# Kernel optimization log

Measured on AMD Instinct MI355X. Metric: run time of the kernel, lower is better.

## Reference

```python
import jax, jax.numpy as jnp
import numpy as np

N = 10000; E = 320000; B = 262144
F_NODE = 64; F_EDGE = 8; H = 4; C = 32
EVO_IN = C * 4 * H + 1      # 513
EVO_HID = 256; EVO_DIM = 64
FLOW_IN = EVO_DIM + 5       # 69
FLOW_HID = 256
SLOPE = 0.01                # torch LeakyReLU default slope
GAT_SLOPE = 0.2             # GATv2 attention LeakyReLU slope
EPS = 1e-5                  # BatchNorm eps


def setup_inputs() -> dict:
    key = jax.random.key(0)
    ks = iter(jax.random.split(key, 64))
    def nrm(shape, scale=1.0):
        return jax.random.normal(next(ks), shape, jnp.float32) * scale
    inp = {}
    inp['x1'] = nrm((N, F_NODE))
    inp['edge_index1'] = jax.random.randint(next(ks), (2, E), 0, N)
    inp['edge_attr1'] = nrm((E, F_EDGE))
    inp['x2'] = nrm((N, F_NODE))
    inp['edge_index2'] = jax.random.randint(next(ks), (2, E), 0, N)
    inp['edge_attr2'] = nrm((E, F_EDGE))
    inp['dist_m'] = jax.random.uniform(next(ks), (N, N), jnp.float32)
    inp['node_visit'] = jax.random.uniform(next(ks), (N, 2), jnp.float32)
    inp['od_nodes'] = jax.random.randint(next(ks), (B, 2), 0, N)
    # GATv2Conv params per snapshot: lin_l, lin_r (bias=True), lin_edge (bias=False), att [H,C], out bias [H*C]
    for p in ('g1', 'g2'):
        s = 1.0 / np.sqrt(F_NODE)
        inp[p + '_Wl'] = nrm((H * C, F_NODE), s)
        inp[p + '_bl'] = jnp.zeros((H * C,), jnp.float32)
        inp[p + '_Wr'] = nrm((H * C, F_NODE), s)
        inp[p + '_br'] = jnp.zeros((H * C,), jnp.float32)
        inp[p + '_We'] = nrm((H * C, F_EDGE), 1.0 / np.sqrt(F_EDGE))
        inp[p + '_att'] = nrm((H, C), 1.0 / np.sqrt(C))
        inp[p + '_bias'] = jnp.zeros((H * C,), jnp.float32)
    # EvoEmbedding (all Linear bias=False)
    inp['e_W1'] = nrm((EVO_HID, EVO_IN), 1.0 / np.sqrt(EVO_IN))
    inp['e_W2'] = nrm((EVO_HID, EVO_HID), 1.0 / np.sqrt(EVO_HID))
    inp['e_W3'] = nrm((EVO_HID, EVO_HID), 1.0 / np.sqrt(EVO_HID))
    inp['e_W4'] = nrm((EVO_HID // 2, EVO_HID), 1.0 / np.sqrt(EVO_HID))
    inp['e_Wout'] = nrm((EVO_DIM, EVO_HID // 2), 1.0 / np.sqrt(EVO_HID // 2))
    # FlowGenerator (Linear bias=False) + BatchNorm affine params
    inp['f_W1'] = nrm((FLOW_HID, FLOW_IN), 1.0 / np.sqrt(FLOW_IN))
    inp['f_W2'] = nrm((FLOW_HID, FLOW_HID), 1.0 / np.sqrt(FLOW_HID))
    inp['f_W3'] = nrm((FLOW_HID, FLOW_HID), 1.0 / np.sqrt(FLOW_HID))
    inp['f_W4'] = nrm((FLOW_HID // 2, FLOW_HID), 1.0 / np.sqrt(FLOW_HID))
    inp['f_Wout'] = nrm((1, FLOW_HID // 2), 1.0 / np.sqrt(FLOW_HID // 2))
    inp['f_g1'] = jnp.ones((FLOW_HID,), jnp.float32);  inp['f_b1'] = jnp.zeros((FLOW_HID,), jnp.float32)
    inp['f_g2'] = jnp.ones((FLOW_HID,), jnp.float32);  inp['f_b2'] = jnp.zeros((FLOW_HID,), jnp.float32)
    inp['f_g3'] = jnp.ones((FLOW_HID,), jnp.float32);  inp['f_b3'] = jnp.zeros((FLOW_HID,), jnp.float32)
    inp['f_g4'] = jnp.ones((FLOW_HID // 2,), jnp.float32); inp['f_b4'] = jnp.zeros((FLOW_HID // 2,), jnp.float32)
    return inp


def _gatv2(x, ei, ea, Wl, bl, Wr, br, We, att, bias):
    src, dst = ei[0], ei[1]
    # self-loops with fill_value='mean': per-target mean of incoming edge_attr
    deg = jax.ops.segment_sum(jnp.ones_like(dst, jnp.float32), dst, N)
    mean_attr = jax.ops.segment_sum(ea, dst, N) / jnp.maximum(deg, 1.0)[:, None]
    loops = jnp.arange(N)
    s = jnp.concatenate([src, loops]); d = jnp.concatenate([dst, loops])
    eaf = jnp.concatenate([ea, mean_attr], axis=0)            # [E+N, F_EDGE]
    xl = (x @ Wl.T + bl).reshape(N, H, C)                     # source transform
    xr = (x @ Wr.T + br).reshape(N, H, C)                     # target transform
    em = (eaf @ We.T).reshape(-1, H, C)
    msg = jax.nn.leaky_relu(xl[s] + xr[d] + em, GAT_SLOPE)    # [E+N, H, C]
    scr = jnp.einsum('ehc,hc->eh', msg, att)                  # [E+N, H]
    mx = jax.ops.segment_max(scr, d, N)
    ex = jnp.exp(scr - mx[d])
    den = jax.ops.segment_sum(ex, d, N)
    alpha = ex / den[d]                                       # softmax over incoming edges
    out = jax.ops.segment_sum(alpha[:, :, None] * xl[s], d, N).reshape(N, H * C) + bias
    return jax.nn.relu(out), alpha


def _evo(v, W1, W2, W3, W4, Wout):
    h = jax.nn.leaky_relu(v @ W1.T, SLOPE)
    h = jax.nn.leaky_relu(h @ W2.T, SLOPE)
    h = jax.nn.leaky_relu(h @ W3.T, SLOPE)
    h = jax.nn.leaky_relu(h @ W4.T, SLOPE)
    return h @ Wout.T


def _bn(x, g, b):
    mu = x.mean(0)
    var = x.var(0)
    return (x - mu) * jax.lax.rsqrt(var + EPS) * g + b


def _flow(v, W1, W2, W3, W4, Wout, g1, b1, g2, b2, g3, b3, g4, b4):
    h = jax.nn.leaky_relu(_bn(v @ W1.T, g1, b1), SLOPE)
    h = jax.nn.leaky_relu(_bn(h @ W2.T, g2, b2), SLOPE)
    h = jax.nn.leaky_relu(_bn(h @ W3.T, g3, b3), SLOPE)
    h = jax.nn.leaky_relu(_bn(h @ W4.T, g4, b4), SLOPE)
    return (h @ Wout.T).squeeze(-1)


def reference(x1, edge_index1, edge_attr1, x2, edge_index2, edge_attr2, dist_m, node_visit, od_nodes,
              g1_Wl, g1_bl, g1_Wr, g1_br, g1_We, g1_att, g1_bias,
              g2_Wl, g2_bl, g2_Wr, g2_br, g2_We, g2_att, g2_bias,
              e_W1, e_W2, e_W3, e_W4, e_Wout,
              f_W1, f_W2, f_W3, f_W4, f_Wout,
              f_g1, f_b1, f_g2, f_b2, f_g3, f_b3, f_g4, f_b4):
    n1, a1 = _gatv2(x1, edge_index1, edge_attr1, g1_Wl, g1_bl, g1_Wr, g1_br, g1_We, g1_att, g1_bias)
    n2, a2 = _gatv2(x2, edge_index2, edge_attr2, g2_Wl, g2_bl, g2_Wr, g2_br, g2_We, g2_att, g2_bias)
    o = od_nodes[:, 0]; dn = od_nodes[:, 1]
    dist = dist_m[o, dn][:, None]                              # fused gather replacing python loop
    feat = jnp.concatenate([n1[o], n1[dn], n2[o], n2[dn], dist], axis=1)  # [B, 513]
    evo = _evo(feat, e_W1, e_W2, e_W3, e_W4, e_Wout)           # [B, EVO_DIM]
    # NOTE: original uses node_visit[:,0] for BOTH o_visit and d_visit (kept faithful)
    ov = node_visit[o, 0:1]; dv = node_visit[dn, 0:1]
    ovn = node_visit[o, 1:2]; dvn = node_visit[dn, 1:2]
    cat = jnp.concatenate([evo, ov, dv, ovn, dvn, dist], axis=1)  # [B, 69]
    inferred = _flow(cat, f_W1, f_W2, f_W3, f_W4, f_Wout, f_g1, f_b1, f_g2, f_b2, f_g3, f_b3, f_g4, f_b4)
    return (inferred, a1, a2, evo)
```

## Files before the change

### kernel.cpp

```cpp
#include <hip/hip_runtime.h>

typedef unsigned short u16;
typedef unsigned int u32;

#define NN 10000
#define NE 320000
#define ET 330000
#define NB 262144

typedef __attribute__((ext_vector_type(8))) short bf16x8;
typedef __attribute__((ext_vector_type(4))) float f32x4;

__device__ __forceinline__ u16 f2b(float f) {
  u32 u = __float_as_uint(f);
  u += 0x7fffu + ((u >> 16) & 1u);
  return (u16)(u >> 16);
}
__device__ __forceinline__ float b2f(u16 h) {
  return __uint_as_float(((u32)h) << 16);
}
__device__ __forceinline__ float lrelu(float v, float s) { return v > 0.f ? v : v * s; }

__device__ __forceinline__ void g2lds16(const void* g, void* l) {
  __builtin_amdgcn_global_load_lds((const __attribute__((address_space(1))) void*)g,
                                   (__attribute__((address_space(3))) void*)l, 16, 0, 0);
}

__global__ __launch_bounds__(256) void k_prep(const float* __restrict__ eW2, const float* __restrict__ eW3,
                                              const float* __restrict__ eW4, const float* __restrict__ eWo,
                                              const float* __restrict__ fW1, const float* __restrict__ fW2,
                                              const float* __restrict__ fW3, const float* __restrict__ fW4,
                                              const float* __restrict__ eW1,
                                              u16* eW2b, u16* eW3b, u16* eW4b, u16* eWob,
                                              u16* fW2b, u16* fW3b, u16* fW4b,
                                              float* W1T, float* w512, u16* combW) {
  const int blk = blockIdx.x, tid = threadIdx.x;
  if (blk < 256) {
    int t = blk * 256 + tid; eW2b[t] = f2b(eW2[t]);
  } else if (blk < 512) {
    int t = (blk - 256) * 256 + tid; eW3b[t] = f2b(eW3[t]);
  } else if (blk < 640) {
    int t = (blk - 512) * 256 + tid; eW4b[t] = f2b(eW4[t]);
  } else if (blk < 672) {
    int t = (blk - 640) * 256 + tid; eWob[t] = f2b(eWo[t]);
  } else if (blk < 928) {
    int t = (blk - 672) * 256 + tid; fW2b[t] = f2b(fW2[t]);
  } else if (blk < 1184) {
    int t = (blk - 928) * 256 + tid; fW3b[t] = f2b(fW3[t]);
  } else if (blk < 1312) {
    int t = (blk - 1184) * 256 + tid; fW4b[t] = f2b(fW4[t]);
  } else if (blk < 1568) {
    int m = blk - 1312;
    for (int k = tid; k < 512; k += 256) W1T[(size_t)k * 256 + m] = eW1[(size_t)m * 513 + k];
  } else if (blk == 1568) {
    w512[tid] = eW1[(size_t)tid * 513 + 512];
  } else {
    int m = blk - 1569;
    int k = tid;
    if (k < 160) {
      float v = 0.f;
      if (k < 128) {
        const float* fr = fW1 + (size_t)m * 69;
        for (int j = 0; j < 64; ++j) v += fr[j] * eWo[(size_t)j * 128 + k];
      } else if (k < 133) {
        v = fW1[(size_t)m * 69 + 64 + (k - 128)];
      }
      combW[(size_t)m * 160 + k] = f2b(v);
    }
  }
}

__global__ __launch_bounds__(256) void k_sprep(const int* __restrict__ od, const float* __restrict__ dm,
                                               const float* __restrict__ nv,
                                               float* __restrict__ distb, u16* __restrict__ bufC) {
  int b = blockIdx.x * 256 + threadIdx.x;
  int o = od[b * 2], d = od[b * 2 + 1];
  float dist = dm[(size_t)o * NN + d];
  distb[b] = dist;
  u16 tmp[32];
  tmp[0] = f2b(nv[o * 2]);
  tmp[1] = f2b(nv[d * 2]);
  tmp[2] = f2b(nv[o * 2 + 1]);
  tmp[3] = f2b(nv[d * 2 + 1]);
  tmp[4] = f2b(dist);
#pragma unroll
  for (int k = 5; k < 32; ++k) tmp[k] = 0;
  u16* p = bufC + (size_t)b * 160 + 128;
#pragma unroll
  for (int k = 0; k < 4; ++k) *(bf16x8*)(p + k * 8) = *(bf16x8*)(tmp + k * 8);
}

__global__ __launch_bounds__(256) void k_count(const int* __restrict__ ei, int* __restrict__ cnt) {
  int t = blockIdx.x * 256 + threadIdx.x;
  if (t >= ET) return;
  int d = (t < NE) ? ei[NE + t] : (t - NE);
  atomicAdd(&cnt[d], 1);
}

__global__ __launch_bounds__(1024) void k_scan(const int* __restrict__ cnt, int* __restrict__ cs) {
  __shared__ int part[1024];
  int tid = threadIdx.x;
  int base = tid * 10;
  int local[10];
  int s = 0;
#pragma unroll
  for (int i = 0; i < 10; ++i) {
    int idx = base + i;
    int v = (idx < NN) ? cnt[idx] : 0;
    local[i] = s; s += v;
  }
  part[tid] = s;
  __syncthreads();
  for (int off = 1; off < 1024; off <<= 1) {
    int v = (tid >= off) ? part[tid - off] : 0;
    __syncthreads();
    part[tid] += v;
    __syncthreads();
  }
  int pre = (tid > 0) ? part[tid - 1] : 0;
#pragma unroll
  for (int i = 0; i < 10; ++i) {
    int idx = base + i;
    if (idx < NN) cs[idx] = pre + local[i];
  }
  if (tid == 1023) cs[NN] = part[1023];
}

__global__ __launch_bounds__(256) void k_fill(const int* __restrict__ ei, const int* __restrict__ cs,
                                              int* __restrict__ wr, int2* __restrict__ csr) {
  int t = blockIdx.x * 256 + threadIdx.x;
  if (t >= ET) return;
  int s, d;
  if (t < NE) { s = ei[t]; d = ei[NE + t]; } else { s = t - NE; d = s; }
  int pos = atomicAdd(&wr[d], 1);
  csr[cs[d] + pos] = make_int2(t, s);
}

__global__ __launch_bounds__(256) void k_asum(const int2* __restrict__ csr, const int* __restrict__ cs,
                                              const float* __restrict__ ea, float* __restrict__ asum) {
  int wid = (blockIdx.x * 256 + threadIdx.x) >> 6;
  int lane = threadIdx.x & 63;
  int beg = cs[wid], end = cs[wid + 1];
  int j = lane & 7, slot = lane >> 3;
  float acc = 0.f;
  for (int i = beg + slot; i < end; i += 8) {
    int e = csr[i].x;
    if (e < NE) acc += ea[(size_t)e * 8 + j];
  }
  acc += __shfl_xor(acc, 8);
  acc += __shfl_xor(acc, 16);
  acc += __shfl_xor(acc, 32);
  if (lane < 8) {
    float dr = (float)(end - beg - 1);
    asum[(size_t)wid * 8 + lane] = acc / fmaxf(dr, 1.f);
  }
}

__global__ __launch_bounds__(256) void k_xlr(const float* __restrict__ x,
                                             const float* __restrict__ Wl, const float* __restrict__ bl,
                                             const float* __restrict__ Wr, const float* __restrict__ br,
                                             float* __restrict__ xl, float* __restrict__ xr) {
  __shared__ float sx[128];
  int nb = blockIdx.x * 2;
  for (int i = threadIdx.x; i < 128; i += 256) sx[i] = x[(size_t)nb * 64 + i];
  __syncthreads();
  int half = threadIdx.x >> 7;
  int node = nb + half;
  int m = threadIdx.x & 127;
  const float* xv = sx + (half << 6);
  float al = bl[m], ar = br[m];
  const float* wl = Wl + (size_t)m * 64;
  const float* wr = Wr + (size_t)m * 64;
#pragma unroll 8
  for (int k = 0; k < 64; ++k) { float xk = xv[k]; al += xk * wl[k]; ar += xk * wr[k]; }
  xl[(size_t)node * 128 + m] = al;
  xr[(size_t)node * 128 + m] = ar;
}

__global__ __launch_bounds__(256) void k_scr(const float* __restrict__ xl, const float* __restrict__ xr,
                                             const int* __restrict__ ei, const float* __restrict__ ea,
                                             const float* __restrict__ mattr,
                                             const float* __restrict__ We, const float* __restrict__ att,
                                             float* __restrict__ scr) {
  const int lane = threadIdx.x & 63;
  const int sub = lane & 31;
  const int half = lane >> 5;
  float4 w0[4], w1[4];
#pragma unroll
  for (int c = 0; c < 4; ++c) {
    const float* wp = We + (size_t)(sub * 4 + c) * 8;
    w0[c] = *(const float4*)wp;
    w1[c] = *(const float4*)(wp + 4);
  }
  const float4 attv = *(const float4*)(att + sub * 4);
  const int gw = (blockIdx.x * 256 + threadIdx.x) >> 6;
  const int nw = gridDim.x * 4;
  for (int p = gw; p < ET / 2; p += nw) {
    int e = p * 2 + half;
    int s, d; const float* ap;
    if (e < NE) { s = ei[e]; d = ei[NE + e]; ap = ea + (size_t)e * 8; }
    else { s = e - NE; d = s; ap = mattr + (size_t)(e - NE) * 8; }
    float4 a0 = *(const float4*)ap;
    float4 a1 = *(const float4*)(ap + 4);
    float4 xlv = *(const float4*)(xl + (size_t)s * 128 + sub * 4);
    float4 xrv = *(const float4*)(xr + (size_t)d * 128 + sub * 4);
    const float* xle = (const float*)&xlv;
    const float* xre = (const float*)&xrv;
    const float* ate = (const float*)&attv;
    float psum = 0.f;
#pragma unroll
    for (int c = 0; c < 4; ++c) {
      float em = a0.x * w0[c].x + a0.y * w0[c].y + a0.z * w0[c].z + a0.w * w0[c].w
               + a1.x * w1[c].x + a1.y * w1[c].y + a1.z * w1[c].z + a1.w * w1[c].w;
      float v = xle[c] + xre[c] + em;
      v = v > 0.f ? v : 0.2f * v;
      psum += v * ate[c];
    }
    psum += __shfl_xor(psum, 1);
    psum += __shfl_xor(psum, 2);
    psum += __shfl_xor(psum, 4);
    if ((sub & 7) == 0) scr[(size_t)e * 4 + (sub >> 3)] = psum;
  }
}

__global__ __launch_bounds__(256) void k_nodered(const float* __restrict__ scr, const int2* __restrict__ csr,
                                                 const int* __restrict__ cs, const float* __restrict__ xl,
                                                 const float* __restrict__ bias,
                                                 float* __restrict__ m_out, float* __restrict__ den_out,
                                                 float* __restrict__ nout) {
  int d = (blockIdx.x * 256 + threadIdx.x) >> 6;
  int lane = threadIdx.x & 63;
  int h0 = lane >> 5;
  int beg = cs[d], end = cs[d + 1];
  float mx0 = -3.4e38f, mx1 = -3.4e38f;
  for (int i = beg; i < end; ++i) {
    int e = csr[i].x;
    mx0 = fmaxf(mx0, scr[(size_t)e * 4 + h0]);
    mx1 = fmaxf(mx1, scr[(size_t)e * 4 + h0 + 2]);
  }
  float acc0 = 0.f, acc1 = 0.f, dn0 = 0.f, dn1 = 0.f;
  for (int i = beg; i < end; ++i) {
    int2 es = csr[i];
    float ex0 = __expf(scr[(size_t)es.x * 4 + h0] - mx0);
    float ex1 = __expf(scr[(size_t)es.x * 4 + h0 + 2] - mx1);
    dn0 += ex0; dn1 += ex1;
    const float* xp = xl + (size_t)es.y * 128;
    acc0 += ex0 * xp[lane];
    acc1 += ex1 * xp[64 + lane];
  }
  if (lane == 0 || lane == 32) {
    m_out[d * 4 + h0] = mx0;     m_out[d * 4 + h0 + 2] = mx1;
    den_out[d * 4 + h0] = dn0;   den_out[d * 4 + h0 + 2] = dn1;
  }
  nout[(size_t)d * 128 + lane] = fmaxf(acc0 / dn0 + bias[lane], 0.f);
  nout[(size_t)d * 128 + 64 + lane] = fmaxf(acc1 / dn1 + bias[64 + lane], 0.f);
}

__global__ __launch_bounds__(256) void k_alpha(const float* __restrict__ scr, const int* __restrict__ ei,
                                               const float* __restrict__ m, const float* __restrict__ den,
                                               float* __restrict__ aout) {
  int t = blockIdx.x * 256 + threadIdx.x;
  if (t >= ET * 4) return;
  int e = t >> 2, h = t & 3;
  int d = (e < NE) ? ei[NE + e] : (e - NE);
  aout[t] = __expf(scr[t] - m[d * 4 + h]) / den[d * 4 + h];
}

__global__ __launch_bounds__(256) void k_qtab(const float* __restrict__ n1, const float* __restrict__ n2,
                                              const float* __restrict__ W1T,
                                              u16* __restrict__ Qo, u16* __restrict__ Qd) {
  __shared__ float s1[2048], s2[2048];
  int nb = blockIdx.x * 16;
  for (int i = threadIdx.x; i < 2048; i += 256) {
    s1[i] = n1[(size_t)nb * 128 + i];
    s2[i] = n2[(size_t)nb * 128 + i];
  }
  __syncthreads();
  int m = threadIdx.x;
  float qo[16], qd[16];
#pragma unroll
  for (int i = 0; i < 16; ++i) { qo[i] = 0.f; qd[i] = 0.f; }
#pragma unroll 2
  for (int k = 0; k < 128; ++k) {
    float w0 = W1T[(size_t)k * 256 + m];
    float w1 = W1T[(size_t)(128 + k) * 256 + m];
    float w2 = W1T[(size_t)(256 + k) * 256 + m];
    float w3 = W1T[(size_t)(384 + k) * 256 + m];
#pragma unroll
    for (int i = 0; i < 16; ++i) {
      float a = s1[i * 128 + k], b = s2[i * 128 + k];
      qo[i] += a * w0 + b * w2;
      qd[i] += a * w1 + b * w3;
    }
  }
#pragma unroll
  for (int i = 0; i < 16; ++i) {
    Qo[(size_t)(nb + i) * 256 + m] = f2b(qo[i]);
    Qd[(size_t)(nb + i) * 256 + m] = f2b(qd[i]);
  }
}

__global__ __launch_bounds__(256) void k_evo1(const u16* __restrict__ Qo, const u16* __restrict__ Qd,
                                              const int* __restrict__ od, const float* __restrict__ distb,
                                              const float* __restrict__ w512, u16* __restrict__ h1) {
  __shared__ float sw[256];
  sw[threadIdx.x] = w512[threadIdx.x];
  __syncthreads();
  int t = blockIdx.x * 256 + threadIdx.x;
  int b = t >> 5, mq = (t & 31) << 3;
  int o = od[b * 2], d = od[b * 2 + 1];
  float dist = distb[b];
  bf16x8 qa = *(const bf16x8*)(Qo + (size_t)o * 256 + mq);
  bf16x8 qc = *(const bf16x8*)(Qd + (size_t)d * 256 + mq);
  bf16x8 r;
#pragma unroll
  for (int j = 0; j < 8; ++j) {
    float v = b2f((u16)qa[j]) + b2f((u16)qc[j]) + dist * sw[mq + j];
    r[j] = (short)f2b(lrelu(v, 0.01f));
  }
  *(bf16x8*)(h1 + (size_t)b * 256 + mq) = r;
}

template <int NF, int EPI, int BNA>
__global__ __launch_bounds__(512) void gemm256(const u16* __restrict__ A, const u16* __restrict__ W,
                                               int K, size_t lda,
                                               u16* __restrict__ obf, int ld_bf,
                                               float* __restrict__ stats,
                                               const float* __restrict__ stin, const float* __restrict__ gg,
                                               const float* __restrict__ bb, float invB) {
  constexpr int M = NF * 64;
  constexpr int CPW = 2 + NF / 2;
  __shared__ alignas(16) u16 Alds[2][256 * 32];
  __shared__ alignas(16) u16 Blds[2][M * 32];
  __shared__ float sS[256], sT[256];
  const int tid = threadIdx.x;
  const int lane = tid & 63;
  const int w = tid >> 6;
  const int wr = w >> 2, wc = w & 3;
  const size_t rowBase = (size_t)blockIdx.x * 256;

  if (BNA) {
    for (int c = tid; c < K; c += 512) {
      float mu = stin[c] * invB;
      float var = stin[K + c] * invB - mu * mu;
      float sc = rsqrtf(var + 1e-5f) * gg[c];
      sS[c] = sc;
      sT[c] = bb[c] - mu * sc;
    }
    __syncthreads();
  }

  f32x4 acc[8][NF];
  const f32x4 z4 = {0.f, 0.f, 0.f, 0.f};
#pragma unroll
  for (int m = 0; m < 8; ++m)
#pragma unroll
    for (int n = 0; n < NF; ++n) acc[m][n] = z4;

  const int crow = lane >> 2;
  const int ccol = (lane & 3) << 3;
  const int KT = K >> 5;

  auto stage = [&](int buf, int kb) {
#pragma unroll
    for (int i = 0; i < CPW; ++i) {
      const int c = w * CPW + i;
      if (c < 16) {
        const u16* src = A + (rowBase + (c << 4) + crow) * lda + kb + ccol;
        g2lds16(src, &Alds[buf][(c << 4) << 5]);
      } else {
        const u16* src = W + (size_t)(((c - 16) << 4) + crow) * K + kb + ccol;
        g2lds16(src, &Blds[buf][((c - 16) << 4) << 5]);
      }
    }
  };

  stage(0, 0);
  int cur = 0;
  const int lr = lane & 15, lk = (lane >> 4) << 3;
  for (int kt = 0; kt < KT; ++kt) {
    const int kb = kt << 5;
    if (kt + 1 < KT) {
      stage(cur ^ 1, kb + 32);
      if constexpr (NF == 4)
        asm volatile("s_waitcnt vmcnt(4)" ::: "memory");
      else
        asm volatile("s_waitcnt vmcnt(3)" ::: "memory");
    } else {
      asm volatile("s_waitcnt vmcnt(0)" ::: "memory");
    }
    __builtin_amdgcn_s_barrier();

    float sv[8], tv[8];
    if (BNA) {
      float4 s0 = *(const float4*)&sS[kb + lk];
      float4 s1 = *(const float4*)&sS[kb + lk + 4];
      float4 t0 = *(const float4*)&sT[kb + lk];
      float4 t1 = *(const float4*)&sT[kb + lk + 4];
      sv[0] = s0.x; sv[1] = s0.y; sv[2] = s0.z; sv[3] = s0.w;
      sv[4] = s1.x; sv[5] = s1.y; sv[6] = s1.z; sv[7] = s1.w;
      tv[0] = t0.x; tv[1] = t0.y; tv[2] = t0.z; tv[3] = t0.w;
      tv[4] = t1.x; tv[5] = t1.y; tv[6] = t1.z; tv[7] = t1.w;
    }
    bf16x8 bfr[NF];
#pragma unroll
    for (int n = 0; n < NF; ++n)
      bfr[n] = *(const bf16x8*)&Blds[cur][((((wc * NF + n) << 4) + lr) << 5) + lk];
#pragma unroll
    for (int m = 0; m < 8; ++m) {
      bf16x8 af = *(const bf16x8*)&Alds[cur][(((wr << 7) + (m << 4) + lr) << 5) + lk];
      if (BNA) {
        bf16x8 o;
#pragma unroll
        for (int j = 0; j < 8; ++j) {
          float v = fmaf(b2f((u16)af[j]), sv[j], tv[j]);
          v = v > 0.f ? v : v * 0.01f;
          o[j] = (short)f2b(v);
        }
        af = o;
      }
#pragma unroll
      for (int n = 0; n < NF; ++n)
        acc[m][n] = __builtin_amdgcn_mfma_f32_16x16x32_bf16(af, bfr[n], acc[m][n], 0, 0, 0);
    }
    __builtin_amdgcn_s_barrier();
    cur ^= 1;
  }

  const int lg = lane >> 4;
  float csm[NF], cq[NF];
#pragma unroll
  for (int n = 0; n < NF; ++n) { csm[n] = 0.f; cq[n] = 0.f; }
#pragma unroll
  for (int m = 0; m < 8; ++m) {
#pragma unroll
    for (int n = 0; n < NF; ++n) {
      const int col = wc * (NF * 16) + (n << 4) + lr;
#pragma unroll
      for (int j = 0; j < 4; ++j) {
        const size_t row = rowBase + (wr << 7) + (m << 4) + (lg << 2) + j;
        float v = acc[m][n][j];
        if (EPI == 0) {
          v = v > 0.f ? v : v * 0.01f;
          obf[row * ld_bf + col] = f2b(v);
        } else {
          obf[row * ld_bf + col] = f2b(v);
          csm[n] += v; cq[n] += v * v;
        }
      }
    }
  }
  if (EPI == 1) {
#pragma unroll
    for (int n = 0; n < NF; ++n) {
      float s = csm[n], q = cq[n];
      s += __shfl_xor(s, 16); s += __shfl_xor(s, 32);
      q += __shfl_xor(q, 16); q += __shfl_xor(q, 32);
      if (lane < 16) {
        const int col = wc * (NF * 16) + (n << 4) + lane;
        atomicAdd(&stats[col], s);
        atomicAdd(&stats[M + col], q);
      }
    }
  }
}

template <int NF>
__global__ __launch_bounds__(256) void gemm_f32out(const u16* __restrict__ A, const u16* __restrict__ W,
                                                   int K, size_t lda, int M, float* __restrict__ of32) {
  constexpr int CW = NF * 16;
  __shared__ alignas(16) u16 Alds[2][128 * 32];
  __shared__ alignas(16) u16 Blds[2][CW * 2 * 32];
  const int lane = threadIdx.x & 63;
  const int w = threadIdx.x >> 6;
  const int wr = w >> 1, wc = w & 1;
  const size_t rowBase = (size_t)blockIdx.x * 128;

  f32x4 acc[4][NF];
  const f32x4 z4 = {0.f, 0.f, 0.f, 0.f};
#pragma unroll
  for (int m = 0; m < 4; ++m)
#pragma unroll
    for (int n = 0; n < NF; ++n) acc[m][n] = z4;

  const int sr = (w << 4) + (lane >> 2);
  const int sc = (lane & 3) << 3;
  const int KT = K >> 5;

  auto stage = [&](int buf, int kb) {
#pragma unroll
    for (int i = 0; i < 2; ++i) {
      const u16* src = A + (rowBase + (i << 6) + sr) * lda + kb + sc;
      g2lds16(src, &Alds[buf][((i << 6) + (w << 4)) << 5]);
    }
#pragma unroll
    for (int i = 0; i < NF / 2; ++i) {
      const u16* src = W + (size_t)((i << 6) + sr) * K + kb + sc;
      g2lds16(src, &Blds[buf][((i << 6) + (w << 4)) << 5]);
    }
  };

  stage(0, 0);
  int cur = 0;
  for (int kt = 0; kt < KT; ++kt) {
    if (kt + 1 < KT) {
      stage(cur ^ 1, (kt + 1) << 5);
      asm volatile("s_waitcnt vmcnt(3)" ::: "memory");
    } else {
      asm volatile("s_waitcnt vmcnt(0)" ::: "memory");
    }
    __builtin_amdgcn_s_barrier();
    const int lr = lane & 15, lk = (lane >> 4) << 3;
    bf16x8 af[4], bfr[NF];
#pragma unroll
    for (int m = 0; m < 4; ++m)
      af[m] = *(const bf16x8*)&Alds[cur][(((wr << 6) + (m << 4) + lr) << 5) + lk];
#pragma unroll
    for (int n = 0; n < NF; ++n)
      bfr[n] = *(const bf16x8*)&Blds[cur][((wc * CW + (n << 4) + lr) << 5) + lk];
#pragma unroll
    for (int m = 0; m < 4; ++m)
#pragma unroll
      for (int n = 0; n < NF; ++n)
        acc[m][n] = __builtin_amdgcn_mfma_f32_16x16x32_bf16(af[m], bfr[n], acc[m][n], 0, 0, 0);
    __builtin_amdgcn_s_barrier();
    cur ^= 1;
  }

  const int lr = lane & 15, lg = lane >> 4;
#pragma unroll
  for (int m = 0; m < 4; ++m) {
#pragma unroll
    for (int n = 0; n < NF; ++n) {
      const int col = wc * CW + (n << 4) + lr;
      if (col >= M) continue;
#pragma unroll
      for (int j = 0; j < 4; ++j) {
        const size_t row = rowBase + (wr << 6) + (m << 4) + (lg << 2) + j;
        of32[row * M + col] = acc[m][n][j];
      }
    }
  }
}

__global__ __launch_bounds__(256) void k_fout4(const u16* __restrict__ pre, const float* __restrict__ st,
                                               const float* __restrict__ g, const float* __restrict__ b,
                                               const float* __restrict__ W, float* __restrict__ out,
                                               float invB) {
  __shared__ float smu[128], srs[128], sg[128], sb[128], sw[128];
  if (threadIdx.x < 128) {
    int c = threadIdx.x;
    float mu = st[c] * invB;
    float var = st[128 + c] * invB - mu * mu;
    smu[c] = mu;
    srs[c] = rsqrtf(var + 1e-5f);
    sg[c] = g[c];
    sb[c] = b[c];
    sw[c] = W[c];
  }
  __syncthreads();
  int bi = blockIdx.x * 256 + threadIdx.x;
  const u16* hp = pre + (size_t)bi * 128;
  float acc = 0.f;
#pragma unroll
  for (int k = 0; k < 128; k += 8) {
    bf16x8 u = *(const bf16x8*)(hp + k);
#pragma unroll
    for (int j = 0; j < 8; ++j) {
      int c = k + j;
      float v = (b2f((u16)u[j]) - smu[c]) * srs[c] * sg[c] + sb[c];
      v = b2f(f2b(lrelu(v, 0.01f)));
      acc += v * sw[c];
    }
  }
  out[bi] = acc;
}

extern "C" void kernel_launch(void* const* d_in, const int* in_sizes, int n_in,
                              void* d_out, int out_size, void* d_ws, size_t ws_size,
                              hipStream_t stream) {
  (void)in_sizes; (void)n_in; (void)out_size; (void)ws_size;

  const float* x[2] = {(const float*)d_in[0], (const float*)d_in[3]};
  const int* ei[2] = {(const int*)d_in[1], (const int*)d_in[4]};
  const float* ea[2] = {(const float*)d_in[2], (const float*)d_in[5]};
  const float* dm = (const float*)d_in[6];
  const float* nv = (const float*)d_in[7];
  const int* od = (const int*)d_in[8];
  const float* Wl[2] = {(const float*)d_in[9], (const float*)d_in[16]};
  const float* bl[2] = {(const float*)d_in[10], (const float*)d_in[17]};
  const float* Wr[2] = {(const float*)d_in[11], (const float*)d_in[18]};
  const float* br[2] = {(const float*)d_in[12], (const float*)d_in[19]};
  const float* We[2] = {(const float*)d_in[13], (const float*)d_in[20]};
  const float* att[2] = {(const float*)d_in[14], (const float*)d_in[21]};
  const float* bia[2] = {(const float*)d_in[15], (const float*)d_in[22]};
  const float* eW1 = (const float*)d_in[23];
  const float* eW2 = (const float*)d_in[24];
  const float* eW3 = (const float*)d_in[25];
  const float* eW4 = (const float*)d_in[26];
  const float* eWo = (const float*)d_in[27];
  const float* fW1 = (const float*)d_in[28];
  const float* fW2 = (const float*)d_in[29];
  const float* fW3 = (const float*)d_in[30];
  const float* fW4 = (const float*)d_in[31];
  const float* fWo = (const float*)d_in[32];
  const float* fg[4] = {(const float*)d_in[33], (const float*)d_in[35], (const float*)d_in[37], (const float*)d_in[39]};
  const float* fb[4] = {(const float*)d_in[34], (const float*)d_in[36], (const float*)d_in[38], (const float*)d_in[40]};

  float* out_inf = (float*)d_out;
  float* out_a1 = out_inf + NB;
  float* out_a2 = out_a1 + (size_t)ET * 4;
  float* out_evo = out_a2 + (size_t)ET * 4;

  char* base = (char*)d_ws;
  size_t cur = 0;
  auto carve = [&](size_t bytes) -> char* {
    char* p = base + cur;
    cur += (bytes + 255) & ~(size_t)255;
    return p;
  };
  u16* bufA = (u16*)carve((size_t)NB * 256 * 2);
  u16* bufB = (u16*)carve((size_t)NB * 256 * 2);
  u16* bufC = (u16*)carve((size_t)NB * 160 * 2);
  float* n1 = (float*)carve((size_t)NN * 128 * 4);
  float* n2 = (float*)carve((size_t)NN * 128 * 4);
  u16* Qob = (u16*)carve((size_t)NN * 256 * 2);
  u16* Qdb = (u16*)carve((size_t)NN * 256 * 2);
  float* xl = (float*)carve((size_t)NN * 128 * 4);
  float* xr = (float*)carve((size_t)NN * 128 * 4);
  int* cnt = (int*)carve((size_t)(NN + 1) * 4);
  int* wr = (int*)carve((size_t)NN * 4);
  int* cs = (int*)carve((size_t)(NN + 1) * 4);
  int2* csr = (int2*)carve((size_t)ET * 8);
  float* m_out = (float*)carve((size_t)NN * 4 * 4);
  float* den_out = (float*)carve((size_t)NN * 4 * 4);
  float* asum = (float*)carve((size_t)NN * 8 * 4);
  float* scr = (float*)carve((size_t)ET * 4 * 4);
  float* distb = (float*)carve((size_t)NB * 4);
  float* w512 = (float*)carve(1024);
  float* W1T = (float*)carve(512 * 256 * 4);
  float* stats = (float*)carve(1792 * 4);
  float* st[4] = {stats, stats + 512, stats + 1024, stats + 1536};
  u16* eW2b = (u16*)carve(256 * 256 * 2);
  u16* eW3b = (u16*)carve(256 * 256 * 2);
  u16* eW4b = (u16*)carve(128 * 256 * 2);
  u16* eWob = (u16*)carve(64 * 128 * 2);
  u16* fW2b = (u16*)carve(256 * 256 * 2);
  u16* fW3b = (u16*)carve(256 * 256 * 2);
  u16* fW4b = (u16*)carve(128 * 256 * 2);
  u16* combW = (u16*)carve(256 * 160 * 2);

  k_prep<<<1825, 256, 0, stream>>>(eW2, eW3, eW4, eWo, fW1, fW2, fW3, fW4, eW1,
                                   eW2b, eW3b, eW4b, eWob, fW2b, fW3b, fW4b,
                                   W1T, w512, combW);
  hipMemsetAsync(stats, 0, 1792 * 4, stream);
  k_sprep<<<NB / 256, 256, 0, stream>>>(od, dm, nv, distb, bufC);

  float* nout[2] = {n1, n2};
  float* aout[2] = {out_a1, out_a2};
  const int EB = (ET + 255) / 256;
  const size_t cwSpan = (size_t)((char*)wr - (char*)cnt) + (size_t)NN * 4;
  for (int gi = 0; gi < 2; ++gi) {
    hipMemsetAsync(cnt, 0, cwSpan, stream);
    k_count<<<EB, 256, 0, stream>>>(ei[gi], cnt);
    k_scan<<<1, 1024, 0, stream>>>(cnt, cs);
    k_fill<<<EB, 256, 0, stream>>>(ei[gi], cs, wr, csr);
    k_asum<<<NN / 4, 256, 0, stream>>>(csr, cs, ea[gi], asum);
    k_xlr<<<NN / 2, 256, 0, stream>>>(x[gi], Wl[gi], bl[gi], Wr[gi], br[gi], xl, xr);
    k_scr<<<2048, 256, 0, stream>>>(xl, xr, ei[gi], ea[gi], asum, We[gi], att[gi], scr);
    k_nodered<<<NN / 4, 256, 0, stream>>>(scr, csr, cs, xl, bia[gi], m_out, den_out, nout[gi]);
    k_alpha<<<(ET * 4 + 255) / 256, 256, 0, stream>>>(scr, ei[gi], m_out, den_out, aout[gi]);
  }

  k_qtab<<<NN / 16, 256, 0, stream>>>(n1, n2, W1T, Qob, Qdb);
  k_evo1<<<NB * 32 / 256, 256, 0, stream>>>(Qob, Qdb, od, distb, w512, bufA);

  const float invB = 1.0f / (float)NB;
  const int GB = NB / 256;
  gemm256<4, 0, 0><<<GB, 512, 0, stream>>>(bufA, eW2b, 256, 256, bufB, 256, nullptr, nullptr, nullptr, nullptr, 0.f);
  gemm256<4, 0, 0><<<GB, 512, 0, stream>>>(bufB, eW3b, 256, 256, bufA, 256, nullptr, nullptr, nullptr, nullptr, 0.f);
  gemm256<2, 0, 0><<<GB, 512, 0, stream>>>(bufA, eW4b, 256, 256, bufC, 160, nullptr, nullptr, nullptr, nullptr, 0.f);
  gemm_f32out<2><<<NB / 128, 256, 0, stream>>>(bufC, eWob, 128, 160, 64, out_evo);

  gemm256<4, 1, 0><<<GB, 512, 0, stream>>>(bufC, combW, 160, 160, bufA, 256, st[0], nullptr, nullptr, nullptr, 0.f);
  gemm256<4, 1, 1><<<GB, 512, 0, stream>>>(bufA, fW2b, 256, 256, bufB, 256, st[1], st[0], fg[0], fb[0], invB);
  gemm256<4, 1, 1><<<GB, 512, 0, stream>>>(bufB, fW3b, 256, 256, bufA, 256, st[2], st[1], fg[1], fb[1], invB);
  gemm256<2, 1, 1><<<GB, 512, 0, stream>>>(bufA, fW4b, 256, 256, bufB, 128, st[3], st[2], fg[2], fb[2], invB);
  k_fout4<<<NB / 256, 256, 0, stream>>>(bufB, st[3], fg[3], fb[3], fWo, out_inf, invB);
}
```

Before: 1.389 ms.

## Fuse evo layer-1 gather into GEMM and merge tail GEMMs into one kernel

Removes the standalone k_evo1 kernel. The first evo GEMM now gathers Qo/Qd rows through od indices, adds dist*w512, applies LeakyReLU and writes the A tile to LDS directly. The eW4, eWout and combined flow-W1 GEMMs are merged into one k_tail kernel that keeps the 128x160 hidden tile in LDS, so the bufC round trip is gone. The A operand is now loaded via registers with a two-stage prefetch instead of global_load_lds, which adds register pressure and more complex wait counts.

```diff
diff --git a/kernel.cpp b/kernel.cpp
--- a/kernel.cpp
+++ b/kernel.cpp
@@ -25,6 +25,18 @@
   __builtin_amdgcn_global_load_lds((const __attribute__((address_space(1))) void*)g,
                                    (__attribute__((address_space(3))) void*)l, 16, 0, 0);
 }
+
+template <int N> __device__ __forceinline__ void waitv() {
+  if constexpr (N == 0) asm volatile("s_waitcnt vmcnt(0)" ::: "memory");
+  else if constexpr (N == 1) asm volatile("s_waitcnt vmcnt(1)" ::: "memory");
+  else if constexpr (N == 2) asm volatile("s_waitcnt vmcnt(2)" ::: "memory");
+  else if constexpr (N == 3) asm volatile("s_waitcnt vmcnt(3)" ::: "memory");
+  else if constexpr (N == 4) asm volatile("s_waitcnt vmcnt(4)" ::: "memory");
+  else if constexpr (N == 5) asm volatile("s_waitcnt vmcnt(5)" ::: "memory");
+  else asm volatile("s_waitcnt vmcnt(6)" ::: "memory");
+}
+__device__ __forceinline__ void waitl0() { asm volatile("s_waitcnt lgkmcnt(0)" ::: "memory"); }
+__device__ __forceinline__ void fence() { asm volatile("" ::: "memory"); }
 
 __global__ __launch_bounds__(256) void k_prep(const float* __restrict__ eW2, const float* __restrict__ eW3,
                                               const float* __restrict__ eW4, const float* __restrict__ eWo,
@@ -72,22 +84,19 @@
 
 __global__ __launch_bounds__(256) void k_sprep(const int* __restrict__ od, const float* __restrict__ dm,
                                                const float* __restrict__ nv,
-                                               float* __restrict__ distb, u16* __restrict__ bufC) {
+                                               float* __restrict__ distb, u16* __restrict__ sbuf) {
   int b = blockIdx.x * 256 + threadIdx.x;
   int o = od[b * 2], d = od[b * 2 + 1];
   float dist = dm[(size_t)o * NN + d];
   distb[b] = dist;
-  u16 tmp[32];
-  tmp[0] = f2b(nv[o * 2]);
-  tmp[1] = f2b(nv[d * 2]);
-  tmp[2] = f2b(nv[o * 2 + 1]);
-  tmp[3] = f2b(nv[d * 2 + 1]);
-  tmp[4] = f2b(dist);
-#pragma unroll
-  for (int k = 5; k < 32; ++k) tmp[k] = 0;
-  u16* p = bufC + (size_t)b * 160 + 128;
-#pragma unroll
-  for (int k = 0; k < 4; ++k) *(bf16x8*)(p + k * 8) = *(bf16x8*)(tmp + k * 8);
+  bf16x8 r;
+  r[0] = (short)f2b(nv[o * 2]);
+  r[1] = (short)f2b(nv[d * 2]);
+  r[2] = (short)f2b(nv[o * 2 + 1]);
+  r[3] = (short)f2b(nv[d * 2 + 1]);
+  r[4] = (short)f2b(dist);
+  r[5] = 0; r[6] = 0; r[7] = 0;
+  *(bf16x8*)(sbuf + (size_t)b * 8) = r;
 }
 
 __global__ __launch_bounds__(256) void k_count(const int* __restrict__ ei, int* __restrict__ cnt) {
@@ -300,45 +309,42 @@
   }
 }
 
-__global__ __launch_bounds__(256) void k_evo1(const u16* __restrict__ Qo, const u16* __restrict__ Qd,
-                                              const int* __restrict__ od, const float* __restrict__ distb,
-                                              const float* __restrict__ w512, u16* __restrict__ h1) {
-  __shared__ float sw[256];
-  sw[threadIdx.x] = w512[threadIdx.x];
-  __syncthreads();
-  int t = blockIdx.x * 256 + threadIdx.x;
-  int b = t >> 5, mq = (t & 31) << 3;
-  int o = od[b * 2], d = od[b * 2 + 1];
-  float dist = distb[b];
-  bf16x8 qa = *(const bf16x8*)(Qo + (size_t)o * 256 + mq);
-  bf16x8 qc = *(const bf16x8*)(Qd + (size_t)d * 256 + mq);
-  bf16x8 r;
-#pragma unroll
-  for (int j = 0; j < 8; ++j) {
-    float v = b2f((u16)qa[j]) + b2f((u16)qc[j]) + dist * sw[mq + j];
-    r[j] = (short)f2b(lrelu(v, 0.01f));
-  }
-  *(bf16x8*)(h1 + (size_t)b * 256 + mq) = r;
-}
-
-template <int NF, int EPI, int BNA>
+template <int NF, int EPI, int BNA, int EVO>
 __global__ __launch_bounds__(512) void gemm256(const u16* __restrict__ A, const u16* __restrict__ W,
                                                int K, size_t lda,
                                                u16* __restrict__ obf, int ld_bf,
                                                float* __restrict__ stats,
                                                const float* __restrict__ stin, const float* __restrict__ gg,
-                                               const float* __restrict__ bb, float invB) {
+                                               const float* __restrict__ bb, float invB,
+                                               const u16* __restrict__ Qo, const u16* __restrict__ Qd,
+                                               const int* __restrict__ od, const float* __restrict__ distb,
+                                               const float* __restrict__ w512) {
   constexpr int M = NF * 64;
-  constexpr int CPW = 2 + NF / 2;
+  constexpr int BCW = (NF == 4) ? 2 : 1;
+  constexpr int NA = EVO ? 4 : 2;
   __shared__ alignas(16) u16 Alds[2][256 * 32];
   __shared__ alignas(16) u16 Blds[2][M * 32];
   __shared__ float sS[256], sT[256];
+  __shared__ int sO[256], sD[256];
   const int tid = threadIdx.x;
   const int lane = tid & 63;
   const int w = tid >> 6;
   const int wr = w >> 2, wc = w & 3;
   const size_t rowBase = (size_t)blockIdx.x * 256;
-
+  const int crow = lane >> 2, ccol = (lane & 3) << 3;
+  const int arow = tid >> 1;
+  const int acol = (tid & 1) << 4;
+  const int lr = lane & 15, lk = (lane >> 4) << 3, lg = lane >> 4;
+
+  if (EVO) {
+    if (tid < 256) {
+      int2 p = ((const int2*)od)[rowBase + tid];
+      sO[tid] = p.x; sD[tid] = p.y;
+      sT[tid] = distb[rowBase + tid];
+      sS[tid] = w512[tid];
+    }
+    __syncthreads();
+  }
   if (BNA) {
     for (int c = tid; c < K; c += 512) {
       float mu = stin[c] * invB;
@@ -350,6 +356,41 @@
     __syncthreads();
   }
 
+  auto stageB = [&](int buf, int kb) {
+#pragma unroll
+    for (int i = 0; i < BCW; ++i) {
+      int c = w * BCW + i;
+      const u16* src = W + (size_t)((c << 4) + crow) * K + kb + ccol;
+      g2lds16(src, &Blds[buf][(c << 4) << 5]);
+    }
+  };
+  auto loadA = [&](int kb, bf16x8& r0, bf16x8& r1, bf16x8& r2, bf16x8& r3) {
+    if (EVO) {
+      const u16* qo = Qo + (size_t)sO[arow] * 256 + kb + acol;
+      const u16* qd = Qd + (size_t)sD[arow] * 256 + kb + acol;
+      r0 = *(const bf16x8*)qo; r1 = *(const bf16x8*)(qo + 8);
+      r2 = *(const bf16x8*)qd; r3 = *(const bf16x8*)(qd + 8);
+    } else {
+      const u16* ap = A + (rowBase + arow) * lda + kb + acol;
+      r0 = *(const bf16x8*)ap; r1 = *(const bf16x8*)(ap + 8);
+    }
+  };
+  auto writeA = [&](int buf, int kb, bf16x8 r0, bf16x8 r1, bf16x8 r2, bf16x8 r3) {
+    bf16x8 w0, w1;
+    if (EVO) {
+      float dist = sT[arow];
+#pragma unroll
+      for (int j = 0; j < 8; ++j) {
+        float v = b2f((u16)r0[j]) + b2f((u16)r2[j]) + dist * sS[kb + acol + j];
+        w0[j] = (short)f2b(lrelu(v, 0.01f));
+        float v2 = b2f((u16)r1[j]) + b2f((u16)r3[j]) + dist * sS[kb + acol + 8 + j];
+        w1[j] = (short)f2b(lrelu(v2, 0.01f));
+      }
+    } else { w0 = r0; w1 = r1; }
+    *(bf16x8*)&Alds[buf][arow * 32 + acol] = w0;
+    *(bf16x8*)&Alds[buf][arow * 32 + acol + 8] = w1;
+  };
+
   f32x4 acc[8][NF];
   const f32x4 z4 = {0.f, 0.f, 0.f, 0.f};
 #pragma unroll
@@ -357,55 +398,40 @@
 #pragma unroll
     for (int n = 0; n < NF; ++n) acc[m][n] = z4;
 
-  const int crow = lane >> 2;
-  const int ccol = (lane & 3) << 3;
   const int KT = K >> 5;
-
-  auto stage = [&](int buf, int kb) {
-#pragma unroll
-    for (int i = 0; i < CPW; ++i) {
-      const int c = w * CPW + i;
-      if (c < 16) {
-        const u16* src = A + (rowBase + (c << 4) + crow) * lda + kb + ccol;
-        g2lds16(src, &Alds[buf][(c << 4) << 5]);
-      } else {
-        const u16* src = W + (size_t)(((c - 16) << 4) + crow) * K + kb + ccol;
-        g2lds16(src, &Blds[buf][((c - 16) << 4) << 5]);
-      }
-    }
-  };
-
-  stage(0, 0);
+  bf16x8 p0, p1, p2, p3;
+  {
+    bf16x8 c0, c1, c2, c3;
+    loadA(0, c0, c1, c2, c3);
+    writeA(0, 0, c0, c1, c2, c3);
+  }
+  stageB(0, 0);
+  fence();
+  if (KT > 1) loadA(32, p0, p1, p2, p3);
+  fence();
+  waitv<NA>();
+  waitl0();
+  __builtin_amdgcn_s_barrier();
+
   int cur = 0;
-  const int lr = lane & 15, lk = (lane >> 4) << 3;
   for (int kt = 0; kt < KT; ++kt) {
     const int kb = kt << 5;
-    if (kt + 1 < KT) {
-      stage(cur ^ 1, kb + 32);
-      if constexpr (NF == 4)
-        asm volatile("s_waitcnt vmcnt(4)" ::: "memory");
-      else
-        asm volatile("s_waitcnt vmcnt(3)" ::: "memory");
-    } else {
-      asm volatile("s_waitcnt vmcnt(0)" ::: "memory");
-    }
-    __builtin_amdgcn_s_barrier();
+    const bool hasN = kt + 1 < KT, hasNN = kt + 2 < KT;
+    bf16x8 bfr[NF];
+#pragma unroll
+    for (int n = 0; n < NF; ++n)
+      bfr[n] = *(const bf16x8*)&Blds[cur][((((wc * NF + n) << 4) + lr) << 5) + lk];
+    if (hasN) stageB(cur ^ 1, kb + 32);
+    fence();
+    bf16x8 q0, q1, q2, q3;
+    if (hasNN) loadA(kb + 64, q0, q1, q2, q3);
+    fence();
 
     float sv[8], tv[8];
     if (BNA) {
-      float4 s0 = *(const float4*)&sS[kb + lk];
-      float4 s1 = *(const float4*)&sS[kb + lk + 4];
-      float4 t0 = *(const float4*)&sT[kb + lk];
-      float4 t1 = *(const float4*)&sT[kb + lk + 4];
-      sv[0] = s0.x; sv[1] = s0.y; sv[2] = s0.z; sv[3] = s0.w;
-      sv[4] = s1.x; sv[5] = s1.y; sv[6] = s1.z; sv[7] = s1.w;
-      tv[0] = t0.x; tv[1] = t0.y; tv[2] = t0.z; tv[3] = t0.w;
-      tv[4] = t1.x; tv[5] = t1.y; tv[6] = t1.z; tv[7] = t1.w;
-    }
-    bf16x8 bfr[NF];
-#pragma unroll
-    for (int n = 0; n < NF; ++n)
-      bfr[n] = *(const bf16x8*)&Blds[cur][((((wc * NF + n) << 4) + lr) << 5) + lk];
+#pragma unroll
+      for (int j = 0; j < 8; ++j) { sv[j] = sS[kb + lk + j]; tv[j] = sT[kb + lk + j]; }
+    }
 #pragma unroll
     for (int m = 0; m < 8; ++m) {
       bf16x8 af = *(const bf16x8*)&Alds[cur][(((wr << 7) + (m << 4) + lr) << 5) + lk];
@@ -423,11 +449,17 @@
       for (int n = 0; n < NF; ++n)
         acc[m][n] = __builtin_amdgcn_mfma_f32_16x16x32_bf16(af, bfr[n], acc[m][n], 0, 0, 0);
     }
+    if (hasN) {
+      if (hasNN) waitv<BCW + NA>(); else waitv<BCW>();
+      writeA(cur ^ 1, kb + 32, p0, p1, p2, p3);
+      p0 = q0; p1 = q1; p2 = q2; p3 = q3;
+      if (hasNN) waitv<NA>(); else waitv<0>();
+      waitl0();
+    }
     __builtin_amdgcn_s_barrier();
     cur ^= 1;
   }
 
-  const int lg = lane >> 4;
   float csm[NF], cq[NF];
 #pragma unroll
   for (int n = 0; n < NF; ++n) { csm[n] = 0.f; cq[n] = 0.f; }
@@ -465,79 +497,225 @@
   }
 }
 
-template <int NF>
-__global__ __launch_bounds__(256) void gemm_f32out(const u16* __restrict__ A, const u16* __restrict__ W,
-                                                   int K, size_t lda, int M, float* __restrict__ of32) {
-  constexpr int CW = NF * 16;
-  __shared__ alignas(16) u16 Alds[2][128 * 32];
-  __shared__ alignas(16) u16 Blds[2][CW * 2 * 32];
-  const int lane = threadIdx.x & 63;
-  const int w = threadIdx.x >> 6;
-  const int wr = w >> 1, wc = w & 1;
+__global__ __launch_bounds__(256) void k_tail(const u16* __restrict__ A,
+                                              const u16* __restrict__ W4,
+                                              const u16* __restrict__ Wo,
+                                              const u16* __restrict__ Wc,
+                                              const u16* __restrict__ sbuf,
+                                              float* __restrict__ oevo,
+                                              u16* __restrict__ opre,
+                                              float* __restrict__ stats) {
+  __shared__ alignas(16) u16 hS[128 * 160];
+  __shared__ alignas(16) u16 st0[128 * 32];
+  __shared__ alignas(16) u16 st1[128 * 32];
+  const int tid = threadIdx.x;
+  const int lane = tid & 63;
+  const int w = tid >> 6;
   const size_t rowBase = (size_t)blockIdx.x * 128;
-
-  f32x4 acc[4][NF];
-  const f32x4 z4 = {0.f, 0.f, 0.f, 0.f};
-#pragma unroll
-  for (int m = 0; m < 4; ++m)
-#pragma unroll
-    for (int n = 0; n < NF; ++n) acc[m][n] = z4;
-
-  const int sr = (w << 4) + (lane >> 2);
-  const int sc = (lane & 3) << 3;
-  const int KT = K >> 5;
-
-  auto stage = [&](int buf, int kb) {
-#pragma unroll
-    for (int i = 0; i < 2; ++i) {
-      const u16* src = A + (rowBase + (i << 6) + sr) * lda + kb + sc;
-      g2lds16(src, &Alds[buf][((i << 6) + (w << 4)) << 5]);
-    }
-#pragma unroll
-    for (int i = 0; i < NF / 2; ++i) {
-      const u16* src = W + (size_t)((i << 6) + sr) * K + kb + sc;
-      g2lds16(src, &Blds[buf][((i << 6) + (w << 4)) << 5]);
-    }
-  };
-
-  stage(0, 0);
-  int cur = 0;
-  for (int kt = 0; kt < KT; ++kt) {
-    if (kt + 1 < KT) {
-      stage(cur ^ 1, (kt + 1) << 5);
-      asm volatile("s_waitcnt vmcnt(3)" ::: "memory");
-    } else {
-      asm volatile("s_waitcnt vmcnt(0)" ::: "memory");
-    }
+  const int crow = lane >> 2, ccol = (lane & 3) << 3;
+  const int lr = lane & 15, lg = lane >> 4, lk = lg << 3;
+  const int arow = tid >> 1, acol = (tid & 1) << 4;
+
+  {
+    const int wr = w >> 1, wc = w & 1;
+    f32x4 acc[4][4];
+    const f32x4 z4 = {0.f, 0.f, 0.f, 0.f};
+#pragma unroll
+    for (int m = 0; m < 4; ++m)
+#pragma unroll
+      for (int n = 0; n < 4; ++n) acc[m][n] = z4;
+
+    auto stageB1 = [&](int kb) {
+#pragma unroll
+      for (int i = 0; i < 2; ++i) {
+        int c = w * 2 + i;
+        const u16* src = W4 + (size_t)((c << 4) + crow) * 256 + kb + ccol;
+        g2lds16(src, &st1[(c << 4) << 5]);
+      }
+    };
+    auto loadA1 = [&](int kb, bf16x8& r0, bf16x8& r1) {
+      const u16* ap = A + (rowBase + arow) * 256 + kb + acol;
+      r0 = *(const bf16x8*)ap; r1 = *(const bf16x8*)(ap + 8);
+    };
+
+    bf16x8 p0, p1;
+    {
+      bf16x8 c0, c1;
+      loadA1(0, c0, c1);
+      *(bf16x8*)&st0[arow * 32 + acol] = c0;
+      *(bf16x8*)&st0[arow * 32 + acol + 8] = c1;
+    }
+    stageB1(0);
+    fence();
+    loadA1(32, p0, p1);
+    fence();
+    waitv<2>();
+    waitl0();
     __builtin_amdgcn_s_barrier();
-    const int lr = lane & 15, lk = (lane >> 4) << 3;
-    bf16x8 af[4], bfr[NF];
+
+    for (int kt = 0; kt < 8; ++kt) {
+      const int kb = kt << 5;
+      const bool hasN = kt < 7, hasNN = kt < 6;
+      bf16x8 af[4], bf[4];
+#pragma unroll
+      for (int m = 0; m < 4; ++m)
+        af[m] = *(const bf16x8*)&st0[(((wr << 6) + (m << 4) + lr) << 5) + lk];
+#pragma unroll
+      for (int n = 0; n < 4; ++n)
+        bf[n] = *(const bf16x8*)&st1[(((wc << 6) + (n << 4) + lr) << 5) + lk];
+      waitl0();
+      __builtin_amdgcn_s_barrier();
+      if (hasN) stageB1(kb + 32);
+      fence();
+      bf16x8 q0, q1;
+      if (hasNN) loadA1(kb + 64, q0, q1);
+      fence();
+#pragma unroll
+      for (int m = 0; m < 4; ++m)
+#pragma unroll
+        for (int n = 0; n < 4; ++n)
+          acc[m][n] = __builtin_amdgcn_mfma_f32_16x16x32_bf16(af[m], bf[n], acc[m][n], 0, 0, 0);
+      if (hasN) {
+        if (hasNN) waitv<4>(); else waitv<2>();
+        *(bf16x8*)&st0[arow * 32 + acol] = p0;
+        *(bf16x8*)&st0[arow * 32 + acol + 8] = p1;
+        p0 = q0; p1 = q1;
+        if (hasNN) waitv<2>(); else waitv<0>();
+        waitl0();
+      }
+      __builtin_amdgcn_s_barrier();
+    }
 #pragma unroll
     for (int m = 0; m < 4; ++m)
-      af[m] = *(const bf16x8*)&Alds[cur][(((wr << 6) + (m << 4) + lr) << 5) + lk];
-#pragma unroll
-    for (int n = 0; n < NF; ++n)
-      bfr[n] = *(const bf16x8*)&Blds[cur][((wc * CW + (n << 4) + lr) << 5) + lk];
+#pragma unroll
+      for (int n = 0; n < 4; ++n) {
+        const int col = (wc << 6) + (n << 4) + lr;
+#pragma unroll
+        for (int j = 0; j < 4; ++j) {
+          const int row = (wr << 6) + (m << 4) + (lg << 2) + j;
+          float v = acc[m][n][j];
+          v = v > 0.f ? v : v * 0.01f;
+          hS[row * 160 + col] = f2b(v);
+        }
+      }
+  }
+  if (tid < 128) {
+    bf16x8 s8 = *(const bf16x8*)(sbuf + (rowBase + tid) * 8);
+    *(bf16x8*)&hS[tid * 160 + 128] = s8;
+    bf16x8 z = {0, 0, 0, 0, 0, 0, 0, 0};
+    *(bf16x8*)&hS[tid * 160 + 136] = z;
+    *(bf16x8*)&hS[tid * 160 + 144] = z;
+    *(bf16x8*)&hS[tid * 160 + 152] = z;
+  }
+  waitl0();
+  __builtin_amdgcn_s_barrier();
+
+  {
+#pragma unroll
+    for (int i = 0; i < 4; ++i) {
+      int c = w * 4 + i;
+      const u16* src = Wo + (c << 9) + (lane << 3);
+      g2lds16(src, (c < 8) ? (void*)&st0[c << 9] : (void*)&st1[(c - 8) << 9]);
+    }
+    waitv<0>();
+    __builtin_amdgcn_s_barrier();
+    f32x4 acc[2][4];
+    const f32x4 z4 = {0.f, 0.f, 0.f, 0.f};
+#pragma unroll
+    for (int m = 0; m < 2; ++m)
+#pragma unroll
+      for (int n = 0; n < 4; ++n) acc[m][n] = z4;
+#pragma unroll
+    for (int ks = 0; ks < 4; ++ks) {
+      bf16x8 af[2], bf[4];
+#pragma unroll
+      for (int m = 0; m < 2; ++m)
+        af[m] = *(const bf16x8*)&hS[((w << 5) + (m << 4) + lr) * 160 + (ks << 5) + lk];
+#pragma unroll
+      for (int n = 0; n < 4; ++n) {
+        const u16* bp = (n < 2) ? &st0[((n << 4) + lr) * 128] : &st1[(((n - 2) << 4) + lr) * 128];
+        bf[n] = *(const bf16x8*)(bp + (ks << 5) + lk);
+      }
+#pragma unroll
+      for (int m = 0; m < 2; ++m)
+#pragma unroll
+        for (int n = 0; n < 4; ++n)
+          acc[m][n] = __builtin_amdgcn_mfma_f32_16x16x32_bf16(af[m], bf[n], acc[m][n], 0, 0, 0);
+    }
+#pragma unroll
+    for (int m = 0; m < 2; ++m)
+#pragma unroll
+      for (int n = 0; n < 4; ++n) {
+        const int col = (n << 4) + lr;
+#pragma unroll
+        for (int j = 0; j < 4; ++j) {
+          const int row = (w << 5) + (m << 4) + (lg << 2) + j;
+          oevo[(rowBase + row) * 64 + col] = acc[m][n][j];
+        }
+      }
+    __builtin_amdgcn_s_barrier();
+  }
+
+  {
+    const int wr = w >> 1, wc = w & 1;
+    f32x4 acc[4][8];
+    const f32x4 z4 = {0.f, 0.f, 0.f, 0.f};
 #pragma unroll
     for (int m = 0; m < 4; ++m)
 #pragma unroll
-      for (int n = 0; n < NF; ++n)
-        acc[m][n] = __builtin_amdgcn_mfma_f32_16x16x32_bf16(af[m], bfr[n], acc[m][n], 0, 0, 0);
-    __builtin_amdgcn_s_barrier();
-    cur ^= 1;
-  }
-
-  const int lr = lane & 15, lg = lane >> 4;
-#pragma unroll
-  for (int m = 0; m < 4; ++m) {
-#pragma unroll
-    for (int n = 0; n < NF; ++n) {
-      const int col = wc * CW + (n << 4) + lr;
-      if (col >= M) continue;
-#pragma unroll
-      for (int j = 0; j < 4; ++j) {
-        const size_t row = rowBase + (wr << 6) + (m << 4) + (lg << 2) + j;
-        of32[row * M + col] = acc[m][n][j];
+      for (int n = 0; n < 8; ++n) acc[m][n] = z4;
+    for (int ks = 0; ks < 5; ++ks) {
+      const int kb = ks << 5;
+#pragma unroll
+      for (int i = 0; i < 4; ++i) {
+        int c = w * 4 + i;
+        const u16* src = Wc + (size_t)((c << 4) + crow) * 160 + kb + ccol;
+        g2lds16(src, (c < 8) ? (void*)&st0[(c << 4) << 5] : (void*)&st1[((c - 8) << 4) << 5]);
+      }
+      waitv<0>();
+      __builtin_amdgcn_s_barrier();
+      bf16x8 af[4], bf[8];
+#pragma unroll
+      for (int m = 0; m < 4; ++m)
+        af[m] = *(const bf16x8*)&hS[((wr << 6) + (m << 4) + lr) * 160 + kb + lk];
+#pragma unroll
+      for (int n = 0; n < 8; ++n) {
+        const int br = (n << 4) + lr;
+        const u16* bp = (wc == 0) ? &st0[br << 5] : &st1[br << 5];
+        bf[n] = *(const bf16x8*)(bp + lk);
+      }
+#pragma unroll
+      for (int m = 0; m < 4; ++m)
+#pragma unroll
+        for (int n = 0; n < 8; ++n)
+          acc[m][n] = __builtin_amdgcn_mfma_f32_16x16x32_bf16(af[m], bf[n], acc[m][n], 0, 0, 0);
+      __builtin_amdgcn_s_barrier();
+    }
+    float csm[8], cq[8];
+#pragma unroll
+    for (int n = 0; n < 8; ++n) { csm[n] = 0.f; cq[n] = 0.f; }
+#pragma unroll
+    for (int m = 0; m < 4; ++m)
+#pragma unroll
+      for (int n = 0; n < 8; ++n) {
+        const int col = (wc << 7) + (n << 4) + lr;
+#pragma unroll
+        for (int j = 0; j < 4; ++j) {
+          const size_t row = rowBase + (wr << 6) + (m << 4) + (lg << 2) + j;
+          float v = acc[m][n][j];
+          opre[row * 256 + col] = f2b(v);
+          csm[n] += v; cq[n] += v * v;
+        }
+      }
+#pragma unroll
+    for (int n = 0; n < 8; ++n) {
+      float s = csm[n], q = cq[n];
+      s += __shfl_xor(s, 16); s += __shfl_xor(s, 32);
+      q += __shfl_xor(q, 16); q += __shfl_xor(q, 32);
+      if (lane < 16) {
+        const int col = (wc << 7) + (n << 4) + lane;
+        atomicAdd(&stats[col], s);
+        atomicAdd(&stats[256 + col], q);
       }
     }
   }
@@ -621,7 +799,7 @@
   };
   u16* bufA = (u16*)carve((size_t)NB * 256 * 2);
   u16* bufB = (u16*)carve((size_t)NB * 256 * 2);
-  u16* bufC = (u16*)carve((size_t)NB * 160 * 2);
+  u16* sbuf = (u16*)carve((size_t)NB * 8 * 2);
   float* n1 = (float*)carve((size_t)NN * 128 * 4);
   float* n2 = (float*)carve((size_t)NN * 128 * 4);
   u16* Qob = (u16*)carve((size_t)NN * 256 * 2);
@@ -654,7 +832,7 @@
                                    eW2b, eW3b, eW4b, eWob, fW2b, fW3b, fW4b,
                                    W1T, w512, combW);
   hipMemsetAsync(stats, 0, 1792 * 4, stream);
-  k_sprep<<<NB / 256, 256, 0, stream>>>(od, dm, nv, distb, bufC);
+  k_sprep<<<NB / 256, 256, 0, stream>>>(od, dm, nv, distb, sbuf);
 
   float* nout[2] = {n1, n2};
   float* aout[2] = {out_a1, out_a2};
@@ -673,18 +851,25 @@
   }
 
   k_qtab<<<NN / 16, 256, 0, stream>>>(n1, n2, W1T, Qob, Qdb);
-  k_evo1<<<NB * 32 / 256, 256, 0, stream>>>(Qob, Qdb, od, distb, w512, bufA);
 
   const float invB = 1.0f / (float)NB;
   const int GB = NB / 256;
-  gemm256<4, 0, 0><<<GB, 512, 0, stream>>>(bufA, eW2b, 256, 256, bufB, 256, nullptr, nullptr, nullptr, nullptr, 0.f);
-  gemm256<4, 0, 0><<<GB, 512, 0, stream>>>(bufB, eW3b, 256, 256, bufA, 256, nullptr, nullptr, nullptr, nullptr, 0.f);
-  gemm256<2, 0, 0><<<GB, 512, 0, stream>>>(bufA, eW4b, 256, 256, bufC, 160, nullptr, nullptr, nullptr, nullptr, 0.f);
-  gemm_f32out<2><<<NB / 128, 256, 0, stream>>>(bufC, eWob, 128, 160, 64, out_evo);
-
-  gemm256<4, 1, 0><<<GB, 512, 0, stream>>>(bufC, combW, 160, 160, bufA, 256, st[0], nullptr, nullptr, nullptr, 0.f);
-  gemm256<4, 1, 1><<<GB, 512, 0, stream>>>(bufA, fW2b, 256, 256, bufB, 256, st[1], st[0], fg[0], fb[0], invB);
-  gemm256<4, 1, 1><<<GB, 512, 0, stream>>>(bufB, fW3b, 256, 256, bufA, 256, st[2], st[1], fg[1], fb[1], invB);
-  gemm256<2, 1, 1><<<GB, 512, 0, stream>>>(bufA, fW4b, 256, 256, bufB, 128, st[3], st[2], fg[2], fb[2], invB);
+  gemm256<4, 0, 0, 1><<<GB, 512, 0, stream>>>(nullptr, eW2b, 256, 0, bufA, 256, nullptr,
+                                              nullptr, nullptr, nullptr, 0.f,
+                                              Qob, Qdb, od, distb, w512);
+  gemm256<4, 0, 0, 0><<<GB, 512, 0, stream>>>(bufA, eW3b, 256, 256, bufB, 256, nullptr,
+                                              nullptr, nullptr, nullptr, 0.f,
+                                              nullptr, nullptr, nullptr, nullptr, nullptr);
+  k_tail<<<NB / 128, 256, 0, stream>>>(bufB, eW4b, eWob, combW, sbuf, out_evo, bufA, st[0]);
+
+  gemm256<4, 1, 1, 0><<<GB, 512, 0, stream>>>(bufA, fW2b, 256, 256, bufB, 256, st[1],
+                                              st[0], fg[0], fb[0], invB,
+                                              nullptr, nullptr, nullptr, nullptr, nullptr);
+  gemm256<4, 1, 1, 0><<<GB, 512, 0, stream>>>(bufB, fW3b, 256, 256, bufA, 256, st[2],
+                                              st[1], fg[1], fb[1], invB,
+                                              nullptr, nullptr, nullptr, nullptr, nullptr);
+  gemm256<2, 1, 1, 0><<<GB, 512, 0, stream>>>(bufA, fW4b, 256, 256, bufB, 128, st[3],
+                                              st[2], fg[2], fb[2], invB,
+                                              nullptr, nullptr, nullptr, nullptr, nullptr);
   k_fout4<<<NB / 256, 256, 0, stream>>>(bufB, st[3], fg[3], fb[3], fWo, out_inf, invB);
 }
```

Result: slower. 1.484 ms (+6.8%).
